# Performance work log

Hardware: AMD Instinct MI355X
Metric: run time of the kernel (lower is better)

## Reference

```python
import jax, jax.numpy as jnp
import numpy as np

NUM_CLASSES = 80
STRIDES = (8, 16, 32)


def _decode(p, stride):
    # p: [B, 5+C, H, W] raw head -> [B, HW, 5+C] decoded (xy in px, wh=exp*stride)
    B, C, H, W = p.shape
    ys, xs = jnp.meshgrid(jnp.arange(H), jnp.arange(W), indexing='ij')
    grid = jnp.stack([xs, ys], -1).reshape(H * W, 2).astype(p.dtype)
    out = p.reshape(B, C, H * W).transpose(0, 2, 1)
    xy = (out[..., :2] + grid) * stride
    wh = jnp.exp(out[..., 2:4]) * stride
    out = jnp.concatenate([xy, wh, out[..., 4:]], -1)
    es = jnp.full((H * W,), float(stride), p.dtype)
    return out, grid[:, 0], grid[:, 1], es


def _pairwise_iou(gt, pr):
    # gt [G,4] cxcywh, pr [A,4] -> [G,A]
    gt_tl = gt[:, None, :2] - gt[:, None, 2:] * 0.5
    gt_br = gt[:, None, :2] + gt[:, None, 2:] * 0.5
    pr_tl = pr[None, :, :2] - pr[None, :, 2:] * 0.5
    pr_br = pr[None, :, :2] + pr[None, :, 2:] * 0.5
    tl = jnp.maximum(gt_tl, pr_tl)
    br = jnp.minimum(gt_br, pr_br)
    en = jnp.all(tl < br, -1).astype(gt.dtype)
    inter = jnp.prod(br - tl, -1) * en
    a_gt = jnp.prod(gt[:, 2:], -1)[:, None]
    a_pr = jnp.prod(pr[:, 2:], -1)[None, :]
    return inter / (a_gt + a_pr - inter + 1e-16)


def _assign(gt_boxes, gt_cls, bbox, clsp, objp, xg, yg, es):
    # SimOTA assignment for one image (all fixed-shape; non-candidate anchors
    # are masked out via huge cost instead of boolean gather).
    G = gt_boxes.shape[0]
    xc = (xg + 0.5) * es  # [A] anchor centers
    yc = (yg + 0.5) * es
    gl = gt_boxes[:, 0:1] - 0.5 * gt_boxes[:, 2:3]
    gr = gt_boxes[:, 0:1] + 0.5 * gt_boxes[:, 2:3]
    gt_ = gt_boxes[:, 1:2] - 0.5 * gt_boxes[:, 3:4]
    gb = gt_boxes[:, 1:2] + 0.5 * gt_boxes[:, 3:4]
    in_box = (xc[None] > gl) & (xc[None] < gr) & (yc[None] > gt_) & (yc[None] < gb)  # [G,A]
    r = 2.5 * es[None]
    in_ctr = ((xc[None] > gt_boxes[:, 0:1] - r) & (xc[None] < gt_boxes[:, 0:1] + r)
              & (yc[None] > gt_boxes[:, 1:2] - r) & (yc[None] < gt_boxes[:, 1:2] + r))
    fg_cand = jnp.any(in_box, 0) | jnp.any(in_ctr, 0)  # [A]
    in_both = in_box & in_ctr  # [G,A]

    ious = _pairwise_iou(gt_boxes, bbox)  # [G,A]
    ious_m = jnp.where(fg_cand[None, :], ious, 0.0)
    iou_cost = -jnp.log(ious_m + 1e-8)

    # pairwise cls BCE cost: bce(sqrt(sigmoid(cls)*sigmoid(obj)), onehot(gt)).sum(-1)
    p = jnp.sqrt(jax.nn.sigmoid(clsp) * jax.nn.sigmoid(objp[:, None]))  # [A,C]
    lp = jnp.maximum(jnp.log(p), -100.0)
    l1p = jnp.maximum(jnp.log1p(-p), -100.0)
    t = jax.nn.one_hot(gt_cls, NUM_CLASSES, dtype=p.dtype)  # [G,C]
    cls_cost = -(jnp.einsum('ac,gc->ga', lp - l1p, t) + jnp.sum(l1p, -1)[None, :])

    cost = (cls_cost + 3.0 * iou_cost
            + 1e5 * (~in_both).astype(p.dtype)
            + 1e9 * (~fg_cand)[None, :].astype(p.dtype))

    # dynamic-k: k_g = clamp(sum(top10 ious), min=1)
    topk_ious, _ = jax.lax.top_k(ious_m, 10)
    dyn_k = jnp.clip(topk_ious.sum(-1).astype(jnp.int32), 1, None)  # [G]
    rank = jnp.argsort(jnp.argsort(cost, axis=1), axis=1)  # rank of each anchor per gt
    matching = (rank < dyn_k[:, None]) & fg_cand[None, :]  # [G,A]
    # resolve anchors matched to multiple gts: keep min-cost gt
    multi = matching.sum(0) > 1
    best = jnp.argmin(cost, 0)
    matching = jnp.where(multi[None, :], jnp.arange(G)[:, None] == best[None, :], matching)

    fg = jnp.any(matching, 0)  # [A]
    matched_gt = jnp.argmax(matching, 0)  # [A]
    pred_iou = jnp.sum(matching * ious, 0)  # [A]
    matched_cls = gt_cls[matched_gt]
    return fg, matched_gt, pred_iou, matched_cls


def _giou_loss(b, g):
    tl = jnp.maximum(b[..., :2] - b[..., 2:] * 0.5, g[..., :2] - g[..., 2:] * 0.5)
    br = jnp.minimum(b[..., :2] + b[..., 2:] * 0.5, g[..., :2] + g[..., 2:] * 0.5)
    area_b = jnp.prod(b[..., 2:], -1)
    area_g = jnp.prod(g[..., 2:], -1)
    en = jnp.all(tl < br, -1).astype(b.dtype)
    inter = jnp.prod(br - tl, -1) * en
    union = area_b + area_g - inter
    iou = inter / (union + 1e-16)
    ctl = jnp.minimum(b[..., :2] - b[..., 2:] * 0.5, g[..., :2] - g[..., 2:] * 0.5)
    cbr = jnp.maximum(b[..., :2] + b[..., 2:] * 0.5, g[..., :2] + g[..., 2:] * 0.5)
    area_c = jnp.maximum(jnp.prod(cbr - ctl, -1), 1e-16)
    giou = iou - (area_c - union) / area_c
    return 1.0 - jnp.clip(giou, -1.0, 1.0)


def _bce_logits(x, t):
    return jnp.maximum(x, 0.0) - x * t + jnp.log1p(jnp.exp(-jnp.abs(x)))


def _forward(p8, p16, p32, labels):
    outs, xo, yo, eo = [], [], [], []
    for p, s in zip((p8, p16, p32), STRIDES):
        o, x, y, e = _decode(p, s)
        outs.append(o); xo.append(x); yo.append(y); eo.append(e)
    outputs = jnp.concatenate(outs, 1)  # [B, A, 5+C]
    xg = jnp.concatenate(xo); yg = jnp.concatenate(yo); es = jnp.concatenate(eo)

    bbox = outputs[..., :4]
    obj = outputs[..., 4]
    cls = outputs[..., 5:]
    gt_boxes = labels[..., :4]
    gt_cls = labels[..., 4].astype(jnp.int32)

    # assignment runs under no_grad in torch
    det = jax.lax.stop_gradient(outputs)
    fg, matched_gt, pred_iou, matched_cls = jax.vmap(
        lambda gb, gc, o: _assign(gb, gc, o[..., :4], o[..., 5:], o[..., 4], xg, yg, es)
    )(gt_boxes, gt_cls, det)

    fgf = fg.astype(outputs.dtype)  # [B,A]
    reg_t = jnp.take_along_axis(gt_boxes, matched_gt[..., None], axis=1)  # [B,A,4]
    cls_t = (jax.nn.one_hot(matched_cls, NUM_CLASSES, dtype=outputs.dtype)
             * pred_iou[..., None] * fgf[..., None])

    loss_iou = jnp.sum(_giou_loss(bbox, reg_t) * fgf)
    loss_obj = jnp.sum(_bce_logits(obj, fgf))
    loss_cls = jnp.sum(_bce_logits(cls, cls_t) * fgf[..., None])
    num_fg = jnp.maximum(jnp.sum(fgf), 1.0)
    return (5.0 * loss_iou + loss_obj + loss_cls) / num_fg


def setup_inputs() -> dict:
    key = jax.random.key(0)
    k1, k2, k3, k4, k5, k6 = jax.random.split(key, 6)
    B, NGT = 32, 20
    p8 = jax.random.normal(k1, (B, 5 + NUM_CLASSES, 80, 80), dtype=jnp.float32)
    p16 = jax.random.normal(k2, (B, 5 + NUM_CLASSES, 40, 40), dtype=jnp.float32)
    p32 = jax.random.normal(k3, (B, 5 + NUM_CLASSES, 20, 20), dtype=jnp.float32)
    cxy = jax.random.uniform(k4, (B, NGT, 2), dtype=jnp.float32, minval=32.0, maxval=608.0)
    wh = jax.random.uniform(k5, (B, NGT, 2), dtype=jnp.float32, minval=16.0, maxval=128.0)
    cls = jax.random.randint(k6, (B, NGT, 1), 0, NUM_CLASSES).astype(jnp.float32)
    labels = jnp.concatenate([cxy, wh, cls], -1)
    return {"p8": p8, "p16": p16, "p32": p32, "labels": labels}


def reference(p8, p16, p32, labels):
    return _forward(p8, p16, p32, labels)
```

## Files before the change

### kernel.cpp

```cpp
#include <hip/hip_runtime.h>
#include <cstdint>
#include <cstddef>

#define NA 8400
#define NAP 8448
#define NB 32
#define NG 20
#define NCL 80
#define NBLK 33

__device__ __forceinline__ float frcp(float x) { return __builtin_amdgcn_rcpf(x); }
__device__ __forceinline__ float bce0(float x) {
  return fmaxf(x, 0.0f) + __logf(1.0f + __expf(-fabsf(x)));
}

__device__ __forceinline__ void anchor_info(int a, const float* p8, const float* p16,
                                            const float* p32, int b, const float*& base,
                                            int& hw, int& HW, int& xg, int& yg, float& fs) {
  if (a < 6400)      { hw = a;        HW = 6400; xg = hw % 80; yg = hw / 80; fs = 8.f;
                       base = p8  + (size_t)b * 85 * 6400; }
  else if (a < 8000) { hw = a - 6400; HW = 1600; xg = hw % 40; yg = hw / 40; fs = 16.f;
                       base = p16 + (size_t)b * 85 * 1600; }
  else               { hw = a - 8000; HW = 400;  xg = hw % 20; yg = hw / 20; fs = 32.f;
                       base = p32 + (size_t)b * 85 * 400; }
}

__device__ __forceinline__ float iou_raw(float gx, float gy, float gw, float gh, float4 p) {
  float gtlx = gx - gw * 0.5f, gtly = gy - gh * 0.5f;
  float gbrx = gx + gw * 0.5f, gbry = gy + gh * 0.5f;
  float ptlx = p.x - p.z * 0.5f, ptly = p.y - p.w * 0.5f;
  float pbrx = p.x + p.z * 0.5f, pbry = p.y + p.w * 0.5f;
  float tlx = fmaxf(gtlx, ptlx), tly = fmaxf(gtly, ptly);
  float brx = fminf(gbrx, pbrx), bry = fminf(gbry, pbry);
  float inter = ((tlx < brx) && (tly < bry)) ? (brx - tlx) * (bry - tly) : 0.0f;
  float ag = gw * gh, ap = p.z * p.w;
  return inter * frcp(ag + ap - inter + 1e-16f);
}

__device__ __forceinline__ float giou_loss(float4 bb, float gx, float gy, float gw, float gh) {
  float btlx = bb.x - bb.z * 0.5f, btly = bb.y - bb.w * 0.5f;
  float bbrx = bb.x + bb.z * 0.5f, bbry = bb.y + bb.w * 0.5f;
  float gtlx = gx - gw * 0.5f, gtly = gy - gh * 0.5f;
  float gbrx = gx + gw * 0.5f, gbry = gy + gh * 0.5f;
  float tlx = fmaxf(btlx, gtlx), tly = fmaxf(btly, gtly);
  float brx = fminf(bbrx, gbrx), bry = fminf(bbry, gbry);
  float area_b = bb.z * bb.w, area_g = gw * gh;
  float inter = ((tlx < brx) && (tly < bry)) ? (brx - tlx) * (bry - tly) : 0.0f;
  float uni = area_b + area_g - inter;
  float iou = inter / (uni + 1e-16f);
  float ctlx = fminf(btlx, gtlx), ctly = fminf(btly, gtly);
  float cbrx = fmaxf(bbrx, gbrx), cbry = fmaxf(bbry, gbry);
  float area_c = fmaxf((cbrx - ctlx) * (cbry - ctly), 1e-16f);
  float giou = iou - (area_c - uni) / area_c;
  giou = fminf(fmaxf(giou, -1.0f), 1.0f);
  return 1.0f - giou;
}

__global__ __launch_bounds__(256) void k1(const float* __restrict__ p8,
                                          const float* __restrict__ p16,
                                          const float* __restrict__ p32,
                                          const float* __restrict__ labels,
                                          int* __restrict__ n_fg_cnt,
                                          int* __restrict__ fg_list,
                                          unsigned int* __restrict__ am_c,
                                          float4* __restrict__ bbox_c,
                                          float* __restrict__ lso_c,
                                          unsigned int* __restrict__ match_c,
                                          float* __restrict__ blk_obj) {
  __shared__ float s_gt[NG * 4];
  __shared__ unsigned int s_wcnt[4];
  __shared__ float s_part[4];
  __shared__ unsigned int s_base;
  int blk = blockIdx.x, b = blockIdx.y, tid = threadIdx.x, lane = tid & 63, wid = tid >> 6;

  if (tid < NG) {
    s_gt[tid * 4 + 0] = labels[((size_t)b * NG + tid) * 5 + 0];
    s_gt[tid * 4 + 1] = labels[((size_t)b * NG + tid) * 5 + 1];
    s_gt[tid * 4 + 2] = labels[((size_t)b * NG + tid) * 5 + 2];
    s_gt[tid * 4 + 3] = labels[((size_t)b * NG + tid) * 5 + 3];
  }
  __syncthreads();

  int a = blk * 256 + tid;
  match_c[(size_t)b * NAP + a] = 0u;

  bool fg = false;
  unsigned int msk = 0u;
  float bce_obj = 0.0f, obj = 0.0f;
  const float* base = nullptr; int hw = 0, HW = 0, xg = 0, yg = 0; float fs = 8.f;
  if (a < NA) {
    anchor_info(a, p8, p16, p32, b, base, hw, HW, xg, yg, fs);
    obj = base[4 * HW + hw];
    bce_obj = bce0(obj);
    float xc = ((float)xg + 0.5f) * fs;
    float yc = ((float)yg + 0.5f) * fs;
    float r = 2.5f * fs;
#pragma unroll
    for (int g = 0; g < NG; ++g) {
      float gx = s_gt[g * 4 + 0], gy = s_gt[g * 4 + 1];
      float gw = s_gt[g * 4 + 2], gh = s_gt[g * 4 + 3];
      bool inb = (xc > gx - 0.5f * gw) && (xc < gx + 0.5f * gw) &&
                 (yc > gy - 0.5f * gh) && (yc < gy + 0.5f * gh);
      bool inc = (xc > gx - r) && (xc < gx + r) && (yc > gy - r) && (yc < gy + r);
      fg = fg || inb || inc;
      if (inb && inc) msk |= (1u << g);
    }
  }

  unsigned long long bm = __ballot(fg);
#pragma unroll
  for (int off = 32; off; off >>= 1) bce_obj += __shfl_down(bce_obj, off, 64);
  if (lane == 0) { s_wcnt[wid] = (unsigned int)__popcll(bm); s_part[wid] = bce_obj; }
  __syncthreads();
  if (tid == 0) {
    unsigned int cnt = s_wcnt[0] + s_wcnt[1] + s_wcnt[2] + s_wcnt[3];
    s_base = cnt ? (unsigned int)atomicAdd(&n_fg_cnt[b], (int)cnt) : 0u;
    blk_obj[b * NBLK + blk] = s_part[0] + s_part[1] + s_part[2] + s_part[3];
  }
  __syncthreads();

  if (!fg) return;
  unsigned int pos = s_base;
  for (int w = 0; w < wid; ++w) pos += s_wcnt[w];
  pos += (unsigned int)__popcll(bm & ((1ull << lane) - 1ull));
  size_t bo = (size_t)b * NAP;
  int ci = (int)pos;
  fg_list[bo + ci] = a;
  am_c[bo + ci] = msk;

  float v0 = base[hw];
  float v1 = base[HW + hw];
  float v2 = base[2 * HW + hw];
  float v3 = base[3 * HW + hw];
  bbox_c[bo + ci] = make_float4((v0 + (float)xg) * fs, (v1 + (float)yg) * fs,
                                __expf(v2) * fs, __expf(v3) * fs);
  float uo = __logf(1.0f + __expf(-fabsf(obj)));
  lso_c[bo + ci] = fminf(obj, 0.0f) - uo;
}

__global__ __launch_bounds__(256) void k23(const float* __restrict__ p8,
                                           const float* __restrict__ p16,
                                           const float* __restrict__ p32,
                                           const float* __restrict__ labels,
                                           const int* __restrict__ fg_list,
                                           const int* __restrict__ n_fg,
                                           const float* __restrict__ lso_c,
                                           const unsigned int* __restrict__ am_c,
                                           const float4* __restrict__ bbox_c,
                                           float* __restrict__ sb_c,
                                           float2* __restrict__ ct_tbl) {
  __shared__ float s_gt[NG * 4];
  __shared__ int   s_gcls[NG];
  __shared__ float s_sl[8][33];
  __shared__ float s_sb[8][33];
  __shared__ float s_slr[32];
  int b = blockIdx.y, tid = threadIdx.x;
  int part = tid >> 5, cl = tid & 31;

  if (tid < NG) {
    s_gt[tid * 4 + 0] = labels[((size_t)b * NG + tid) * 5 + 0];
    s_gt[tid * 4 + 1] = labels[((size_t)b * NG + tid) * 5 + 1];
    s_gt[tid * 4 + 2] = labels[((size_t)b * NG + tid) * 5 + 2];
    s_gt[tid * 4 + 3] = labels[((size_t)b * NG + tid) * 5 + 3];
    s_gcls[tid] = (int)labels[((size_t)b * NG + tid) * 5 + 4];
  }
  __syncthreads();

  int n = n_fg[b];
  size_t bo = (size_t)b * NAP;

  for (int base_ci = blockIdx.x * 32; base_ci < n; base_ci += gridDim.x * 32) {
    int ci = base_ci + cl;
    bool act = ci < n;
    const float* base = nullptr; int hw = 0, HW = 0, xg, yg; float fs;
    float lso = 0.0f, sl = 0.0f, sb = 0.0f;
    if (act) {
      int a = fg_list[bo + ci];
      lso = lso_c[bo + ci];
      anchor_info(a, p8, p16, p32, b, base, hw, HW, xg, yg, fs);
      const float* cb = base + (size_t)(5 + part * 10) * HW + hw;
      float xs[10];
#pragma unroll
      for (int j = 0; j < 10; ++j) xs[j] = cb[(size_t)j * HW];
#pragma unroll
      for (int j = 0; j < 10; ++j) {
        float x = xs[j];
        float u = __logf(1.0f + __expf(-fabsf(x)));
        sb += fmaxf(x, 0.0f) + u;
        float lsx = fminf(x, 0.0f) - u;
        float lpr = 0.5f * (lsx + lso);
        float p   = __expf(lpr);
        sl += fmaxf(__logf(1.0f - p), -100.0f);
      }
    }
    s_sl[part][cl] = sl;
    s_sb[part][cl] = sb;
    __syncthreads();
    if (tid < 32) {
      float tsl = 0.0f, tsb = 0.0f;
#pragma unroll
      for (int q = 0; q < 8; ++q) { tsl += s_sl[q][tid]; tsb += s_sb[q][tid]; }
      s_slr[tid] = tsl;
      if (base_ci + tid < n) sb_c[bo + base_ci + tid] = tsb;
    }
    __syncthreads();
    if (act) {
      float slr = s_slr[cl];
      unsigned int am = am_c[bo + ci];
      float4 pb = bbox_c[bo + ci];
#pragma unroll
      for (int gg = 0; gg < 3; ++gg) {
        int g = part + (gg << 3);
        if (g < NG) {
          int cg = s_gcls[g];
          float x = base[(size_t)(5 + cg) * HW + hw];
          float u = __logf(1.0f + __expf(-fabsf(x)));
          float lsx = fminf(x, 0.0f) - u;
          float lpr = 0.5f * (lsx + lso);
          float p   = __expf(lpr);
          float l1p = fmaxf(__logf(1.0f - p), -100.0f);
          float wv  = fmaxf(lpr, -100.0f) - l1p;
          float iou = iou_raw(s_gt[g * 4 + 0], s_gt[g * 4 + 1],
                              s_gt[g * 4 + 2], s_gt[g * 4 + 3], pb);
          float cst = -(wv + slr) - 3.0f * __logf(iou + 1e-8f);
          if (!((am >> g) & 1u)) cst += 100000.0f;
          ct_tbl[((size_t)b * NG + g) * NAP + ci] = make_float2(cst, iou);
        }
      }
    }
    __syncthreads();
  }
}

__global__ __launch_bounds__(256) void kBCM(const float2* __restrict__ ct_tbl,
                                            const int* __restrict__ n_fg,
                                            unsigned int* __restrict__ match_c) {
  __shared__ float s_wt[4 * 10];
  __shared__ float s_wc[4 * 10];
  __shared__ int   s_wi[4 * 10];
  int g = blockIdx.x, b = blockIdx.y, tid = threadIdx.x;
  int lane = tid & 63, wid = tid >> 6;
  int n = n_fg[b];
  size_t bo = (size_t)b * NAP;
  const float2* __restrict__ row = ct_tbl + ((size_t)b * NG + g) * NAP;

  float t10[10];
  float c10v[10];
  int   c10i[10];
#pragma unroll
  for (int j = 0; j < 10; ++j) { t10[j] = 0.0f; c10v[j] = 3.4e38f; c10i[j] = 0x7fffffff; }

  for (int ci = tid; ci < n; ci += 256) {
    float2 e = row[ci];
    float cst = e.x, iou = e.y;
    if (iou > t10[9]) {
      t10[9] = iou;
#pragma unroll
      for (int q = 9; q > 0; --q) {
        if (t10[q] > t10[q - 1]) { float t = t10[q]; t10[q] = t10[q - 1]; t10[q - 1] = t; }
        else break;
      }
    }
    if (cst < c10v[9] || (cst == c10v[9] && ci < c10i[9])) {
      c10v[9] = cst; c10i[9] = ci;
#pragma unroll
      for (int q = 9; q > 0; --q) {
        if (c10v[q] < c10v[q - 1] ||
            (c10v[q] == c10v[q - 1] && c10i[q] < c10i[q - 1])) {
          float tv = c10v[q]; c10v[q] = c10v[q - 1]; c10v[q - 1] = tv;
          int   ti = c10i[q]; c10i[q] = c10i[q - 1]; c10i[q - 1] = ti;
        } else break;
      }
    }
  }

  for (int r = 0; r < 10; ++r) {
    float v = t10[0];
    float bv = v;
    float cv = c10v[0]; int cix = c10i[0];
    float cbv = cv;     int cbi = cix;
#pragma unroll
    for (int off = 32; off; off >>= 1) {
      bv = fmaxf(bv, __shfl_down(bv, off, 64));
      float ov = __shfl_down(cbv, off, 64);
      int   oi = __shfl_down(cbi, off, 64);
      if (ov < cbv || (ov == cbv && oi < cbi)) { cbv = ov; cbi = oi; }
    }
    bv  = __shfl(bv, 0, 64);
    cbv = __shfl(cbv, 0, 64);
    cbi = __shfl(cbi, 0, 64);
    unsigned long long won = __ballot(v == bv);
    if (lane == __ffsll(won) - 1) {
#pragma unroll
      for (int q = 0; q < 9; ++q) t10[q] = t10[q + 1];
      t10[9] = -1.0f;
    }
    if (cv == cbv && cix == cbi) {
#pragma unroll
      for (int q = 0; q < 9; ++q) { c10v[q] = c10v[q + 1]; c10i[q] = c10i[q + 1]; }
      c10v[9] = 3.4e38f; c10i[9] = 0x7fffffff;
    }
    if (lane == 0) {
      s_wt[wid * 10 + r] = bv;
      s_wc[wid * 10 + r] = cbv;
      s_wi[wid * 10 + r] = cbi;
    }
  }
  __syncthreads();

  if (tid == 0) {
    int p0 = 0, p1 = 0, p2 = 0, p3 = 0;
    float s = 0.0f;
    for (int r = 0; r < 10; ++r) {
      float v0 = (p0 < 10) ? s_wt[p0]      : -2.0f;
      float v1 = (p1 < 10) ? s_wt[10 + p1] : -2.0f;
      float v2 = (p2 < 10) ? s_wt[20 + p2] : -2.0f;
      float v3 = (p3 < 10) ? s_wt[30 + p3] : -2.0f;
      float m = fmaxf(fmaxf(v0, v1), fmaxf(v2, v3));
      s += m;
      if (m == v0) ++p0; else if (m == v1) ++p1; else if (m == v2) ++p2; else ++p3;
    }
    int k = (int)s;
    if (k < 1) k = 1;
    int q[4] = {0, 0, 0, 0};
    for (int it = 0; it < k; ++it) {
      float bv = 3.3e38f; int bi = 0x7fffffff; int sel = -1;
#pragma unroll
      for (int w = 0; w < 4; ++w) {
        if (q[w] < 10) {
          float v = s_wc[w * 10 + q[w]];
          int   i = s_wi[w * 10 + q[w]];
          if (v < bv || (v == bv && i < bi)) { bv = v; bi = i; sel = w; }
        }
      }
      if (sel < 0 || bv >= 1e37f) break;
      atomicOr(&match_c[bo + bi], 1u << g);
      ++q[sel];
    }
  }
}

__global__ __launch_bounds__(256) void kD(const float* __restrict__ p8,
                                          const float* __restrict__ p16,
                                          const float* __restrict__ p32,
                                          const float* __restrict__ labels,
                                          const float2* __restrict__ ct_tbl,
                                          const int* __restrict__ n_fg,
                                          const unsigned int* __restrict__ match_c,
                                          const int* __restrict__ fg_list,
                                          const float4* __restrict__ bbox_c,
                                          const float* __restrict__ sb_c,
                                          const float* __restrict__ blk_obj,
                                          float* __restrict__ accum,
                                          int* __restrict__ done,
                                          float* __restrict__ out) {
  __shared__ float s_gt[NG * 5];
  __shared__ float s_red[16];
  __shared__ int s_flag;
  int b = blockIdx.y, tid = threadIdx.x;
  int n = n_fg[b];
  size_t bo = (size_t)b * NAP;

  if (tid < NG * 5) s_gt[tid] = labels[(size_t)b * NG * 5 + tid];
  __syncthreads();

  float li = 0.0f, oe = 0.0f, lc = 0.0f, nf = 0.0f;
  int ci = blockIdx.x * 256 + tid;
  if (ci < n) {
    unsigned int m = match_c[bo + ci];
    if (m != 0u) {
      int mg;
      if (m & (m - 1)) {
        float bestc = 3.4e38f; mg = 0;
#pragma unroll 4
        for (int gq = 0; gq < NG; ++gq) {
          float cst = ct_tbl[((size_t)b * NG + gq) * NAP + ci].x;
          if (cst < bestc) { bestc = cst; mg = gq; }
        }
      } else {
        mg = __ffs(m) - 1;
      }
      int a = fg_list[bo + ci];
      const float* base; int hw, HW, xg, yg; float fs;
      anchor_info(a, p8, p16, p32, b, base, hw, HW, xg, yg, fs);
      float4 pb = bbox_c[bo + ci];
      float gx = s_gt[mg * 5], gy = s_gt[mg * 5 + 1];
      float gw = s_gt[mg * 5 + 2], gh = s_gt[mg * 5 + 3];
      int cgq = (int)s_gt[mg * 5 + 4];
      float piou = ct_tbl[((size_t)b * NG + mg) * NAP + ci].y;
      li = giou_loss(pb, gx, gy, gw, gh);
      float xcls = base[(size_t)(5 + cgq) * HW + hw];
      lc = sb_c[bo + ci] - xcls * piou;
      oe = base[4 * HW + hw];
      nf = 1.0f;
    }
  }

  float vals[4] = {li, oe, lc, nf};
#pragma unroll
  for (int q2 = 0; q2 < 4; ++q2) {
#pragma unroll
    for (int off = 32; off; off >>= 1) vals[q2] += __shfl_down(vals[q2], off, 64);
  }
  int lane = tid & 63;
  if (lane == 0) {
    int w = tid >> 6;
    s_red[w * 4 + 0] = vals[0];
    s_red[w * 4 + 1] = vals[1];
    s_red[w * 4 + 2] = vals[2];
    s_red[w * 4 + 3] = vals[3];
  }
  __syncthreads();
  if (tid < 4) {
    const int slot[4] = {0, 2, 3, 4};
    float s = s_red[tid] + s_red[4 + tid] + s_red[8 + tid] + s_red[12 + tid];
    if (s != 0.0f) atomicAdd(&accum[slot[tid]], s);
  }
  __syncthreads();

  if (tid == 0) {
    __threadfence();
    s_flag = (atomicAdd(done, 1) == NBLK * NB - 1) ? 1 : 0;
  }
  __syncthreads();
  if (!s_flag) return;

  float s = 0.0f;
  for (int i = tid; i < NB * NBLK; i += 256) s += blk_obj[i];
#pragma unroll
  for (int off = 32; off; off >>= 1) s += __shfl_down(s, off, 64);
  if ((tid & 63) == 0) s_red[tid >> 6] = s;
  __syncthreads();
  if (tid == 0) {
    float obj_base = s_red[0] + s_red[1] + s_red[2] + s_red[3];
    float loss_iou = atomicAdd(&accum[0], 0.0f);
    float oex      = atomicAdd(&accum[2], 0.0f);
    float loss_cls = atomicAdd(&accum[3], 0.0f);
    float num_fg   = atomicAdd(&accum[4], 0.0f);
    float loss_obj = obj_base - oex;
    out[0] = (5.0f * loss_iou + loss_obj + loss_cls) / fmaxf(num_fg, 1.0f);
  }
}

extern "C" void kernel_launch(void* const* d_in, const int* in_sizes, int n_in,
                              void* d_out, int out_size, void* d_ws, size_t ws_size,
                              hipStream_t stream) {
  const float* p8     = (const float*)d_in[0];
  const float* p16    = (const float*)d_in[1];
  const float* p32    = (const float*)d_in[2];
  const float* labels = (const float*)d_in[3];
  float* out = (float*)d_out;

  const size_t BAP = (size_t)NB * NAP;
  char* w = (char*)d_ws;
  float4*       bbox_c   = (float4*)w;
  float2*       ct_tbl   = (float2*)(w + BAP * 16);
  char*         w2       = (char*)ct_tbl + (size_t)NB * NG * NAP * 8;
  int*          fg_list  = (int*)(w2);
  unsigned int* match_c  = (unsigned int*)(w2 + BAP * 4);
  float*        sb_c     = (float*)(w2 + BAP * 8);
  float*        lso_c    = (float*)(w2 + BAP * 12);
  unsigned int* am_c     = (unsigned int*)(w2 + BAP * 16);
  char*         w3       = w2 + BAP * 20;
  int*          n_fg     = (int*)w3;
  float*        accum    = (float*)(w3 + 128);
  int*          done     = (int*)(w3 + 384);
  float*        blk_obj  = (float*)(w3 + 512);

  hipMemsetAsync(w3, 0, 512, stream);

  k1  <<<dim3(NBLK, NB), dim3(256), 0, stream>>>(p8, p16, p32, labels, n_fg, fg_list, am_c,
                                                 bbox_c, lso_c, match_c, blk_obj);
  k23 <<<dim3(NBLK, NB), dim3(256), 0, stream>>>(p8, p16, p32, labels, fg_list, n_fg, lso_c,
                                                 am_c, bbox_c, sb_c, ct_tbl);
  kBCM<<<dim3(NG, NB), dim3(256), 0, stream>>>(ct_tbl, n_fg, match_c);
  kD  <<<dim3(NBLK, NB), dim3(256), 0, stream>>>(p8, p16, p32, labels, ct_tbl, n_fg, match_c,
                                                 fg_list, bbox_c, sb_c, blk_obj, accum,
                                                 done, out);
}
```

Before: 189.7 us.

## Fuse SimOTA pipeline from four kernels into two with per-image assignment block

The candidate-compaction kernel now also computes the pairwise cost/IoU table for its own block's candidates, keeping them in shared memory instead of writing and rereading am/lso/bbox intermediates. Top-k dynamic-k selection and the final loss are merged into one kernel with a 640-thread block per image, which builds the match mask in shared memory. This removes two launches and the global match/am/lso buffers. In exchange, the last stage runs on only 32 blocks with each wave doing serial top-k over two GT rows, which reduces parallelism.

```diff
diff --git a/kernel.cpp b/kernel.cpp
--- a/kernel.cpp
+++ b/kernel.cpp
@@ -56,34 +56,43 @@
   return 1.0f - giou;
 }
 
-__global__ __launch_bounds__(256) void k1(const float* __restrict__ p8,
+__global__ __launch_bounds__(256) void kA(const float* __restrict__ p8,
                                           const float* __restrict__ p16,
                                           const float* __restrict__ p32,
                                           const float* __restrict__ labels,
                                           int* __restrict__ n_fg_cnt,
                                           int* __restrict__ fg_list,
-                                          unsigned int* __restrict__ am_c,
                                           float4* __restrict__ bbox_c,
-                                          float* __restrict__ lso_c,
-                                          unsigned int* __restrict__ match_c,
+                                          float* __restrict__ sb_c,
+                                          float2* __restrict__ ct_tbl,
                                           float* __restrict__ blk_obj) {
   __shared__ float s_gt[NG * 4];
+  __shared__ int   s_gcls[NG];
+  __shared__ int   s_a[256];
+  __shared__ unsigned int s_m[256];
+  __shared__ float s_lso[256];
+  __shared__ float4 s_bb[256];
+  __shared__ float s_sl[8][33];
+  __shared__ float s_sbv[8][33];
+  __shared__ float s_slr[32];
   __shared__ unsigned int s_wcnt[4];
   __shared__ float s_part[4];
   __shared__ unsigned int s_base;
+  __shared__ int s_cnt;
+
   int blk = blockIdx.x, b = blockIdx.y, tid = threadIdx.x, lane = tid & 63, wid = tid >> 6;
+  size_t bo = (size_t)b * NAP;
 
   if (tid < NG) {
     s_gt[tid * 4 + 0] = labels[((size_t)b * NG + tid) * 5 + 0];
     s_gt[tid * 4 + 1] = labels[((size_t)b * NG + tid) * 5 + 1];
     s_gt[tid * 4 + 2] = labels[((size_t)b * NG + tid) * 5 + 2];
     s_gt[tid * 4 + 3] = labels[((size_t)b * NG + tid) * 5 + 3];
+    s_gcls[tid] = (int)labels[((size_t)b * NG + tid) * 5 + 4];
   }
   __syncthreads();
 
   int a = blk * 256 + tid;
-  match_c[(size_t)b * NAP + a] = 0u;
-
   bool fg = false;
   unsigned int msk = 0u;
   float bce_obj = 0.0f, obj = 0.0f;
@@ -114,74 +123,46 @@
   __syncthreads();
   if (tid == 0) {
     unsigned int cnt = s_wcnt[0] + s_wcnt[1] + s_wcnt[2] + s_wcnt[3];
+    s_cnt = (int)cnt;
     s_base = cnt ? (unsigned int)atomicAdd(&n_fg_cnt[b], (int)cnt) : 0u;
     blk_obj[b * NBLK + blk] = s_part[0] + s_part[1] + s_part[2] + s_part[3];
   }
   __syncthreads();
 
-  if (!fg) return;
-  unsigned int pos = s_base;
-  for (int w = 0; w < wid; ++w) pos += s_wcnt[w];
-  pos += (unsigned int)__popcll(bm & ((1ull << lane) - 1ull));
-  size_t bo = (size_t)b * NAP;
-  int ci = (int)pos;
-  fg_list[bo + ci] = a;
-  am_c[bo + ci] = msk;
-
-  float v0 = base[hw];
-  float v1 = base[HW + hw];
-  float v2 = base[2 * HW + hw];
-  float v3 = base[3 * HW + hw];
-  bbox_c[bo + ci] = make_float4((v0 + (float)xg) * fs, (v1 + (float)yg) * fs,
-                                __expf(v2) * fs, __expf(v3) * fs);
-  float uo = __logf(1.0f + __expf(-fabsf(obj)));
-  lso_c[bo + ci] = fminf(obj, 0.0f) - uo;
-}
-
-__global__ __launch_bounds__(256) void k23(const float* __restrict__ p8,
-                                           const float* __restrict__ p16,
-                                           const float* __restrict__ p32,
-                                           const float* __restrict__ labels,
-                                           const int* __restrict__ fg_list,
-                                           const int* __restrict__ n_fg,
-                                           const float* __restrict__ lso_c,
-                                           const unsigned int* __restrict__ am_c,
-                                           const float4* __restrict__ bbox_c,
-                                           float* __restrict__ sb_c,
-                                           float2* __restrict__ ct_tbl) {
-  __shared__ float s_gt[NG * 4];
-  __shared__ int   s_gcls[NG];
-  __shared__ float s_sl[8][33];
-  __shared__ float s_sb[8][33];
-  __shared__ float s_slr[32];
-  int b = blockIdx.y, tid = threadIdx.x;
+  if (fg) {
+    unsigned int li = 0;
+    for (int w = 0; w < wid; ++w) li += s_wcnt[w];
+    li += (unsigned int)__popcll(bm & ((1ull << lane) - 1ull));
+    float v0 = base[hw];
+    float v1 = base[HW + hw];
+    float v2 = base[2 * HW + hw];
+    float v3 = base[3 * HW + hw];
+    float4 bb4 = make_float4((v0 + (float)xg) * fs, (v1 + (float)yg) * fs,
+                             __expf(v2) * fs, __expf(v3) * fs);
+    float uo = __logf(1.0f + __expf(-fabsf(obj)));
+    float lso = fminf(obj, 0.0f) - uo;
+    s_a[li] = a; s_m[li] = msk; s_lso[li] = lso; s_bb[li] = bb4;
+    int ci = (int)(s_base + li);
+    fg_list[bo + ci] = a;
+    bbox_c[bo + ci] = bb4;
+  }
+  __syncthreads();
+
+  int cnt = s_cnt;
   int part = tid >> 5, cl = tid & 31;
-
-  if (tid < NG) {
-    s_gt[tid * 4 + 0] = labels[((size_t)b * NG + tid) * 5 + 0];
-    s_gt[tid * 4 + 1] = labels[((size_t)b * NG + tid) * 5 + 1];
-    s_gt[tid * 4 + 2] = labels[((size_t)b * NG + tid) * 5 + 2];
-    s_gt[tid * 4 + 3] = labels[((size_t)b * NG + tid) * 5 + 3];
-    s_gcls[tid] = (int)labels[((size_t)b * NG + tid) * 5 + 4];
-  }
-  __syncthreads();
-
-  int n = n_fg[b];
-  size_t bo = (size_t)b * NAP;
-
-  for (int base_ci = blockIdx.x * 32; base_ci < n; base_ci += gridDim.x * 32) {
-    int ci = base_ci + cl;
-    bool act = ci < n;
-    const float* base = nullptr; int hw = 0, HW = 0, xg, yg; float fs;
+  for (int t0 = 0; t0 < cnt; t0 += 32) {
+    int idx = t0 + cl;
+    bool act = idx < cnt;
+    const float* base2 = nullptr; int hw2 = 0, HW2 = 0, xg2, yg2; float fs2;
     float lso = 0.0f, sl = 0.0f, sb = 0.0f;
     if (act) {
-      int a = fg_list[bo + ci];
-      lso = lso_c[bo + ci];
-      anchor_info(a, p8, p16, p32, b, base, hw, HW, xg, yg, fs);
-      const float* cb = base + (size_t)(5 + part * 10) * HW + hw;
+      int a2 = s_a[idx];
+      lso = s_lso[idx];
+      anchor_info(a2, p8, p16, p32, b, base2, hw2, HW2, xg2, yg2, fs2);
+      const float* cb = base2 + (size_t)(5 + part * 10) * HW2 + hw2;
       float xs[10];
 #pragma unroll
-      for (int j = 0; j < 10; ++j) xs[j] = cb[(size_t)j * HW];
+      for (int j = 0; j < 10; ++j) xs[j] = cb[(size_t)j * HW2];
 #pragma unroll
       for (int j = 0; j < 10; ++j) {
         float x = xs[j];
@@ -194,26 +175,27 @@
       }
     }
     s_sl[part][cl] = sl;
-    s_sb[part][cl] = sb;
+    s_sbv[part][cl] = sb;
     __syncthreads();
     if (tid < 32) {
       float tsl = 0.0f, tsb = 0.0f;
 #pragma unroll
-      for (int q = 0; q < 8; ++q) { tsl += s_sl[q][tid]; tsb += s_sb[q][tid]; }
+      for (int q = 0; q < 8; ++q) { tsl += s_sl[q][tid]; tsb += s_sbv[q][tid]; }
       s_slr[tid] = tsl;
-      if (base_ci + tid < n) sb_c[bo + base_ci + tid] = tsb;
+      if (t0 + tid < cnt) sb_c[bo + s_base + t0 + tid] = tsb;
     }
     __syncthreads();
     if (act) {
       float slr = s_slr[cl];
-      unsigned int am = am_c[bo + ci];
-      float4 pb = bbox_c[bo + ci];
+      unsigned int am = s_m[idx];
+      float4 pb = s_bb[idx];
+      int ci = (int)(s_base) + idx;
 #pragma unroll
       for (int gg = 0; gg < 3; ++gg) {
         int g = part + (gg << 3);
         if (g < NG) {
           int cg = s_gcls[g];
-          float x = base[(size_t)(5 + cg) * HW + hw];
+          float x = base2[(size_t)(5 + cg) * HW2 + hw2];
           float u = __logf(1.0f + __expf(-fabsf(x)));
           float lsx = fminf(x, 0.0f) - u;
           float lpr = 0.5f * (lsx + lso);
@@ -232,121 +214,12 @@
   }
 }
 
-__global__ __launch_bounds__(256) void kBCM(const float2* __restrict__ ct_tbl,
-                                            const int* __restrict__ n_fg,
-                                            unsigned int* __restrict__ match_c) {
-  __shared__ float s_wt[4 * 10];
-  __shared__ float s_wc[4 * 10];
-  __shared__ int   s_wi[4 * 10];
-  int g = blockIdx.x, b = blockIdx.y, tid = threadIdx.x;
-  int lane = tid & 63, wid = tid >> 6;
-  int n = n_fg[b];
-  size_t bo = (size_t)b * NAP;
-  const float2* __restrict__ row = ct_tbl + ((size_t)b * NG + g) * NAP;
-
-  float t10[10];
-  float c10v[10];
-  int   c10i[10];
-#pragma unroll
-  for (int j = 0; j < 10; ++j) { t10[j] = 0.0f; c10v[j] = 3.4e38f; c10i[j] = 0x7fffffff; }
-
-  for (int ci = tid; ci < n; ci += 256) {
-    float2 e = row[ci];
-    float cst = e.x, iou = e.y;
-    if (iou > t10[9]) {
-      t10[9] = iou;
-#pragma unroll
-      for (int q = 9; q > 0; --q) {
-        if (t10[q] > t10[q - 1]) { float t = t10[q]; t10[q] = t10[q - 1]; t10[q - 1] = t; }
-        else break;
-      }
-    }
-    if (cst < c10v[9] || (cst == c10v[9] && ci < c10i[9])) {
-      c10v[9] = cst; c10i[9] = ci;
-#pragma unroll
-      for (int q = 9; q > 0; --q) {
-        if (c10v[q] < c10v[q - 1] ||
-            (c10v[q] == c10v[q - 1] && c10i[q] < c10i[q - 1])) {
-          float tv = c10v[q]; c10v[q] = c10v[q - 1]; c10v[q - 1] = tv;
-          int   ti = c10i[q]; c10i[q] = c10i[q - 1]; c10i[q - 1] = ti;
-        } else break;
-      }
-    }
-  }
-
-  for (int r = 0; r < 10; ++r) {
-    float v = t10[0];
-    float bv = v;
-    float cv = c10v[0]; int cix = c10i[0];
-    float cbv = cv;     int cbi = cix;
-#pragma unroll
-    for (int off = 32; off; off >>= 1) {
-      bv = fmaxf(bv, __shfl_down(bv, off, 64));
-      float ov = __shfl_down(cbv, off, 64);
-      int   oi = __shfl_down(cbi, off, 64);
-      if (ov < cbv || (ov == cbv && oi < cbi)) { cbv = ov; cbi = oi; }
-    }
-    bv  = __shfl(bv, 0, 64);
-    cbv = __shfl(cbv, 0, 64);
-    cbi = __shfl(cbi, 0, 64);
-    unsigned long long won = __ballot(v == bv);
-    if (lane == __ffsll(won) - 1) {
-#pragma unroll
-      for (int q = 0; q < 9; ++q) t10[q] = t10[q + 1];
-      t10[9] = -1.0f;
-    }
-    if (cv == cbv && cix == cbi) {
-#pragma unroll
-      for (int q = 0; q < 9; ++q) { c10v[q] = c10v[q + 1]; c10i[q] = c10i[q + 1]; }
-      c10v[9] = 3.4e38f; c10i[9] = 0x7fffffff;
-    }
-    if (lane == 0) {
-      s_wt[wid * 10 + r] = bv;
-      s_wc[wid * 10 + r] = cbv;
-      s_wi[wid * 10 + r] = cbi;
-    }
-  }
-  __syncthreads();
-
-  if (tid == 0) {
-    int p0 = 0, p1 = 0, p2 = 0, p3 = 0;
-    float s = 0.0f;
-    for (int r = 0; r < 10; ++r) {
-      float v0 = (p0 < 10) ? s_wt[p0]      : -2.0f;
-      float v1 = (p1 < 10) ? s_wt[10 + p1] : -2.0f;
-      float v2 = (p2 < 10) ? s_wt[20 + p2] : -2.0f;
-      float v3 = (p3 < 10) ? s_wt[30 + p3] : -2.0f;
-      float m = fmaxf(fmaxf(v0, v1), fmaxf(v2, v3));
-      s += m;
-      if (m == v0) ++p0; else if (m == v1) ++p1; else if (m == v2) ++p2; else ++p3;
-    }
-    int k = (int)s;
-    if (k < 1) k = 1;
-    int q[4] = {0, 0, 0, 0};
-    for (int it = 0; it < k; ++it) {
-      float bv = 3.3e38f; int bi = 0x7fffffff; int sel = -1;
-#pragma unroll
-      for (int w = 0; w < 4; ++w) {
-        if (q[w] < 10) {
-          float v = s_wc[w * 10 + q[w]];
-          int   i = s_wi[w * 10 + q[w]];
-          if (v < bv || (v == bv && i < bi)) { bv = v; bi = i; sel = w; }
-        }
-      }
-      if (sel < 0 || bv >= 1e37f) break;
-      atomicOr(&match_c[bo + bi], 1u << g);
-      ++q[sel];
-    }
-  }
-}
-
-__global__ __launch_bounds__(256) void kD(const float* __restrict__ p8,
+__global__ __launch_bounds__(640) void kE(const float* __restrict__ p8,
                                           const float* __restrict__ p16,
                                           const float* __restrict__ p32,
                                           const float* __restrict__ labels,
                                           const float2* __restrict__ ct_tbl,
                                           const int* __restrict__ n_fg,
-                                          const unsigned int* __restrict__ match_c,
                                           const int* __restrict__ fg_list,
                                           const float4* __restrict__ bbox_c,
                                           const float* __restrict__ sb_c,
@@ -354,46 +227,122 @@
                                           float* __restrict__ accum,
                                           int* __restrict__ done,
                                           float* __restrict__ out) {
+  __shared__ unsigned int s_mask[NAP];
   __shared__ float s_gt[NG * 5];
-  __shared__ float s_red[16];
+  __shared__ float s_red[40];
   __shared__ int s_flag;
-  int b = blockIdx.y, tid = threadIdx.x;
+
+  int b = blockIdx.x, tid = threadIdx.x;
+  int lane = tid & 63, wid = tid >> 6;
   int n = n_fg[b];
   size_t bo = (size_t)b * NAP;
 
+  for (int i = tid; i < NAP; i += 640) s_mask[i] = 0u;
   if (tid < NG * 5) s_gt[tid] = labels[(size_t)b * NG * 5 + tid];
   __syncthreads();
 
+#pragma unroll
+  for (int gi = 0; gi < 2; ++gi) {
+    int g = wid * 2 + gi;
+    const float2* __restrict__ row = ct_tbl + ((size_t)b * NG + g) * NAP;
+    float t10[10];
+    float c10v[10];
+    int   c10i[10];
+#pragma unroll
+    for (int j = 0; j < 10; ++j) { t10[j] = 0.0f; c10v[j] = 3.4e38f; c10i[j] = 0x7fffffff; }
+
+    for (int ci = lane; ci < n; ci += 64) {
+      float2 e = row[ci];
+      float cst = e.x, iou = e.y;
+      if (iou > t10[9]) {
+        t10[9] = iou;
+#pragma unroll
+        for (int q = 9; q > 0; --q) {
+          if (t10[q] > t10[q - 1]) { float t = t10[q]; t10[q] = t10[q - 1]; t10[q - 1] = t; }
+          else break;
+        }
+      }
+      if (cst < c10v[9] || (cst == c10v[9] && ci < c10i[9])) {
+        c10v[9] = cst; c10i[9] = ci;
+#pragma unroll
+        for (int q = 9; q > 0; --q) {
+          if (c10v[q] < c10v[q - 1] ||
+              (c10v[q] == c10v[q - 1] && c10i[q] < c10i[q - 1])) {
+            float tv = c10v[q]; c10v[q] = c10v[q - 1]; c10v[q - 1] = tv;
+            int   ti = c10i[q]; c10i[q] = c10i[q - 1]; c10i[q - 1] = ti;
+          } else break;
+        }
+      }
+    }
+
+    float s = 0.0f;
+    for (int r = 0; r < 10; ++r) {
+      float v = t10[0];
+      float bv = v;
+#pragma unroll
+      for (int off = 32; off; off >>= 1) bv = fmaxf(bv, __shfl_down(bv, off, 64));
+      bv = __shfl(bv, 0, 64);
+      s += bv;
+      unsigned long long won = __ballot(v == bv);
+      if (lane == __ffsll(won) - 1) {
+#pragma unroll
+        for (int q = 0; q < 9; ++q) t10[q] = t10[q + 1];
+        t10[9] = -1.0f;
+      }
+    }
+    int k = (int)s;
+    if (k < 1) k = 1;
+
+    for (int it = 0; it < k; ++it) {
+      float cv = c10v[0]; int cix = c10i[0];
+      float cbv = cv;     int cbi = cix;
+#pragma unroll
+      for (int off = 32; off; off >>= 1) {
+        float ov = __shfl_down(cbv, off, 64);
+        int   oi = __shfl_down(cbi, off, 64);
+        if (ov < cbv || (ov == cbv && oi < cbi)) { cbv = ov; cbi = oi; }
+      }
+      cbv = __shfl(cbv, 0, 64);
+      cbi = __shfl(cbi, 0, 64);
+      if (cbv >= 1e37f) break;
+      if (cv == cbv && cix == cbi) {
+        atomicOr(&s_mask[cbi], 1u << g);
+#pragma unroll
+        for (int q = 0; q < 9; ++q) { c10v[q] = c10v[q + 1]; c10i[q] = c10i[q + 1]; }
+        c10v[9] = 3.4e38f; c10i[9] = 0x7fffffff;
+      }
+    }
+  }
+  __syncthreads();
+
   float li = 0.0f, oe = 0.0f, lc = 0.0f, nf = 0.0f;
-  int ci = blockIdx.x * 256 + tid;
-  if (ci < n) {
-    unsigned int m = match_c[bo + ci];
-    if (m != 0u) {
-      int mg;
-      if (m & (m - 1)) {
-        float bestc = 3.4e38f; mg = 0;
+  for (int ci = tid; ci < n; ci += 640) {
+    unsigned int m = s_mask[ci];
+    if (m == 0u) continue;
+    int mg;
+    if (m & (m - 1)) {
+      float bestc = 3.4e38f; mg = 0;
 #pragma unroll 4
-        for (int gq = 0; gq < NG; ++gq) {
-          float cst = ct_tbl[((size_t)b * NG + gq) * NAP + ci].x;
-          if (cst < bestc) { bestc = cst; mg = gq; }
-        }
-      } else {
-        mg = __ffs(m) - 1;
-      }
-      int a = fg_list[bo + ci];
-      const float* base; int hw, HW, xg, yg; float fs;
-      anchor_info(a, p8, p16, p32, b, base, hw, HW, xg, yg, fs);
-      float4 pb = bbox_c[bo + ci];
-      float gx = s_gt[mg * 5], gy = s_gt[mg * 5 + 1];
-      float gw = s_gt[mg * 5 + 2], gh = s_gt[mg * 5 + 3];
-      int cgq = (int)s_gt[mg * 5 + 4];
-      float piou = ct_tbl[((size_t)b * NG + mg) * NAP + ci].y;
-      li = giou_loss(pb, gx, gy, gw, gh);
-      float xcls = base[(size_t)(5 + cgq) * HW + hw];
-      lc = sb_c[bo + ci] - xcls * piou;
-      oe = base[4 * HW + hw];
-      nf = 1.0f;
-    }
+      for (int gq = 0; gq < NG; ++gq) {
+        float cst = ct_tbl[((size_t)b * NG + gq) * NAP + ci].x;
+        if (cst < bestc) { bestc = cst; mg = gq; }
+      }
+    } else {
+      mg = __ffs(m) - 1;
+    }
+    int a = fg_list[bo + ci];
+    const float* base; int hw, HW, xg, yg; float fs;
+    anchor_info(a, p8, p16, p32, b, base, hw, HW, xg, yg, fs);
+    float4 pb = bbox_c[bo + ci];
+    float gx = s_gt[mg * 5], gy = s_gt[mg * 5 + 1];
+    float gw = s_gt[mg * 5 + 2], gh = s_gt[mg * 5 + 3];
+    int cgq = (int)s_gt[mg * 5 + 4];
+    float piou = ct_tbl[((size_t)b * NG + mg) * NAP + ci].y;
+    li += giou_loss(pb, gx, gy, gw, gh);
+    float xcls = base[(size_t)(5 + cgq) * HW + hw];
+    lc += sb_c[bo + ci] - xcls * piou;
+    oe += base[4 * HW + hw];
+    nf += 1.0f;
   }
 
   float vals[4] = {li, oe, lc, nf};
@@ -402,37 +351,39 @@
 #pragma unroll
     for (int off = 32; off; off >>= 1) vals[q2] += __shfl_down(vals[q2], off, 64);
   }
-  int lane = tid & 63;
   if (lane == 0) {
-    int w = tid >> 6;
-    s_red[w * 4 + 0] = vals[0];
-    s_red[w * 4 + 1] = vals[1];
-    s_red[w * 4 + 2] = vals[2];
-    s_red[w * 4 + 3] = vals[3];
+    s_red[wid * 4 + 0] = vals[0];
+    s_red[wid * 4 + 1] = vals[1];
+    s_red[wid * 4 + 2] = vals[2];
+    s_red[wid * 4 + 3] = vals[3];
   }
   __syncthreads();
   if (tid < 4) {
     const int slot[4] = {0, 2, 3, 4};
-    float s = s_red[tid] + s_red[4 + tid] + s_red[8 + tid] + s_red[12 + tid];
+    float s = 0.0f;
+#pragma unroll
+    for (int w = 0; w < 10; ++w) s += s_red[w * 4 + tid];
     if (s != 0.0f) atomicAdd(&accum[slot[tid]], s);
   }
   __syncthreads();
 
   if (tid == 0) {
     __threadfence();
-    s_flag = (atomicAdd(done, 1) == NBLK * NB - 1) ? 1 : 0;
+    s_flag = (atomicAdd(done, 1) == NB - 1) ? 1 : 0;
   }
   __syncthreads();
   if (!s_flag) return;
 
   float s = 0.0f;
-  for (int i = tid; i < NB * NBLK; i += 256) s += blk_obj[i];
+  for (int i = tid; i < NB * NBLK; i += 640) s += blk_obj[i];
 #pragma unroll
   for (int off = 32; off; off >>= 1) s += __shfl_down(s, off, 64);
-  if ((tid & 63) == 0) s_red[tid >> 6] = s;
+  if (lane == 0) s_red[wid] = s;
   __syncthreads();
   if (tid == 0) {
-    float obj_base = s_red[0] + s_red[1] + s_red[2] + s_red[3];
+    float obj_base = 0.0f;
+#pragma unroll
+    for (int w = 0; w < 10; ++w) obj_base += s_red[w];
     float loss_iou = atomicAdd(&accum[0], 0.0f);
     float oex      = atomicAdd(&accum[2], 0.0f);
     float loss_cls = atomicAdd(&accum[3], 0.0f);
@@ -457,11 +408,8 @@
   float2*       ct_tbl   = (float2*)(w + BAP * 16);
   char*         w2       = (char*)ct_tbl + (size_t)NB * NG * NAP * 8;
   int*          fg_list  = (int*)(w2);
-  unsigned int* match_c  = (unsigned int*)(w2 + BAP * 4);
-  float*        sb_c     = (float*)(w2 + BAP * 8);
-  float*        lso_c    = (float*)(w2 + BAP * 12);
-  unsigned int* am_c     = (unsigned int*)(w2 + BAP * 16);
-  char*         w3       = w2 + BAP * 20;
+  float*        sb_c     = (float*)(w2 + BAP * 4);
+  char*         w3       = w2 + BAP * 8;
   int*          n_fg     = (int*)w3;
   float*        accum    = (float*)(w3 + 128);
   int*          done     = (int*)(w3 + 384);
@@ -469,12 +417,8 @@
 
   hipMemsetAsync(w3, 0, 512, stream);
 
-  k1  <<<dim3(NBLK, NB), dim3(256), 0, stream>>>(p8, p16, p32, labels, n_fg, fg_list, am_c,
-                                                 bbox_c, lso_c, match_c, blk_obj);
-  k23 <<<dim3(NBLK, NB), dim3(256), 0, stream>>>(p8, p16, p32, labels, fg_list, n_fg, lso_c,
-                                                 am_c, bbox_c, sb_c, ct_tbl);
-  kBCM<<<dim3(NG, NB), dim3(256), 0, stream>>>(ct_tbl, n_fg, match_c);
-  kD  <<<dim3(NBLK, NB), dim3(256), 0, stream>>>(p8, p16, p32, labels, ct_tbl, n_fg, match_c,
-                                                 fg_list, bbox_c, sb_c, blk_obj, accum,
-                                                 done, out);
-}
+  kA<<<dim3(NBLK, NB), dim3(256), 0, stream>>>(p8, p16, p32, labels, n_fg, fg_list,
+                                               bbox_c, sb_c, ct_tbl, blk_obj);
+  kE<<<dim3(NB), dim3(640), 0, stream>>>(p8, p16, p32, labels, ct_tbl, n_fg, fg_list,
+                                         bbox_c, sb_c, blk_obj, accum, done, out);
+}
```

Result: slower. 244.0 us (+28.6%).
